# Kernel optimization log

Hardware: AMD Instinct MI355X
Metric: run time of the kernel (lower is better)

## Reference

```python
import jax, jax.numpy as jnp
import numpy as np
import math

NEG = -1000000.0


def setup_inputs() -> dict:
    key = jax.random.key(0)
    ks = jax.random.split(key, 8)
    B, S, D = 4, 2048, 1024
    std = 1.0 / math.sqrt(D)
    return {
        "queries": jax.random.normal(ks[0], (B, S, D), jnp.float32),
        "keys": jax.random.normal(ks[1], (B, S, D), jnp.float32),
        "values": jax.random.normal(ks[2], (B, S, D), jnp.float32),
        "valid_len": jax.random.randint(ks[3], (B,), 1, S, dtype=jnp.int64 if jax.config.jax_enable_x64 else jnp.int32),
        "W_q": jax.random.normal(ks[4], (D, D), jnp.float32) * std,
        "W_k": jax.random.normal(ks[5], (D, D), jnp.float32) * std,
        "W_v": jax.random.normal(ks[6], (D, D), jnp.float32) * std,
        "W_o": jax.random.normal(ks[7], (D, D), jnp.float32) * std,
    }


def reference(queries, keys, values, valid_len, W_q, W_k, W_v, W_o):
    NUM_HEADS = 16
    B, S, D = queries.shape
    hd = D // NUM_HEADS

    def split_heads(x):
        # (B, S, D) -> (B, H, S, hd)
        return x.reshape(B, -1, NUM_HEADS, hd).transpose(0, 2, 1, 3)

    # nn.Linear with weight W applies x @ W.T
    q = split_heads(queries @ W_q.T)
    k = split_heads(keys @ W_k.T)
    v = split_heads(values @ W_v.T)

    scale = 1.0 / math.sqrt(hd)
    scores = jnp.einsum('bhqd,bhkd->bhqk', q, k) * scale  # (B, H, Sq, Sk)

    # key-padding mask from valid_len: positions >= valid_len are masked
    kpos = jnp.arange(scores.shape[-1])
    pad_mask = kpos[None, None, None, :] >= valid_len[:, None, None, None]
    scores = jnp.where(pad_mask, NEG, scores)
    attn = jax.nn.softmax(scores, axis=-1)

    out = jnp.einsum('bhqk,bhkd->bhqd', attn, v)  # (B, H, Sq, hd)
    out = out.transpose(0, 2, 1, 3).reshape(B, -1, D)
    return out @ W_o.T
```

## Files before the change

kernel.cpp:

```cpp
#include <hip/hip_runtime.h>
#include <hip/hip_bf16.h>

using bf16_t = __bf16;
using bf16x8 = __attribute__((ext_vector_type(8))) __bf16;
using bf16x4 = __attribute__((ext_vector_type(4))) __bf16;
using f32x4  = __attribute__((ext_vector_type(4))) float;

#define S_  2048
#define D_  1024

typedef __attribute__((address_space(1))) unsigned int glb_u32;
typedef __attribute__((address_space(3))) unsigned int lds_u32;

__device__ __forceinline__ void async_cp16(const void* g, void* lds) {
    __builtin_amdgcn_global_load_lds(
        (glb_u32*)(unsigned long long)g,
        (lds_u32*)(unsigned int)(unsigned long long)lds,
        16, 0, 0);
}

__global__ __launch_bounds__(256) void cast4_f32_bf16(const float* __restrict__ a, const float* __restrict__ b,
                                                      const float* __restrict__ c, const float* __restrict__ dd,
                                                      bf16_t* __restrict__ oa, bf16_t* __restrict__ ob,
                                                      bf16_t* __restrict__ oc, bf16_t* __restrict__ od, int n4) {
    int i = blockIdx.x * 256 + threadIdx.x;
    if (i >= n4) return;
    const float* s; bf16_t* d;
    int w = blockIdx.y;
    if      (w == 0) { s = a;  d = oa; }
    else if (w == 1) { s = b;  d = ob; }
    else if (w == 2) { s = c;  d = oc; }
    else             { s = dd; d = od; }
    float4 f = reinterpret_cast<const float4*>(s)[i];
    bf16x4 o;
    o[0] = (bf16_t)f.x; o[1] = (bf16_t)f.y; o[2] = (bf16_t)f.z; o[3] = (bf16_t)f.w;
    reinterpret_cast<bf16x4*>(d)[i] = o;
}

__global__ __launch_bounds__(256, 4) void qkv_gemm(const float* __restrict__ qf,
                                                   const float* __restrict__ kf,
                                                   const float* __restrict__ vf,
                                                   const bf16_t* __restrict__ Wqb,
                                                   const bf16_t* __restrict__ Wkb,
                                                   const bf16_t* __restrict__ Wvb,
                                                   bf16_t* __restrict__ Qp,
                                                   bf16_t* __restrict__ Kp,
                                                   bf16_t* __restrict__ Vt,
                                                   float cs) {
    __shared__ bf16_t As[2][128 * 32];
    __shared__ bf16_t Bs[3][128 * 32];
    const int K = 1024;
    int tid  = threadIdx.x;
    int lane = tid & 63;
    int w    = tid >> 6;
    int l15  = lane & 15, quad = lane >> 4;

    int bid = blockIdx.x;
    int xcd = bid & 7, idx = bid >> 3;
    int z   = idx >> 6;
    int rem = idx & 63;
    int m0 = (xcd * 8 + (rem & 7)) * 128;
    int n0 = (rem >> 3) * 128;
    int wm = (w >> 1) * 64, wn = (w & 1) * 64;

    const float*  Af; const bf16_t* Bt;
    if      (z == 0) { Af = qf; Bt = Wqb; }
    else if (z == 1) { Af = kf; Bt = Wkb; }
    else             { Af = vf; Bt = Wvb; }
    float scale = (z == 0) ? cs : 1.0f;

    const float* Ag = Af + (size_t)(m0 + (tid >> 2)) * K + (tid & 3) * 8;

    int arow = tid >> 2, aslot = tid & 3;
    int aoff = arow * 32 + ((aslot ^ ((arow >> 1) & 3)) * 8);

    const bf16_t* bSrc[2]; int bOff[2];
#pragma unroll
    for (int j = 0; j < 2; j++) {
        int linear = j * 256 + tid;
        int row = linear >> 2, s = linear & 3;
        bSrc[j] = Bt + (size_t)(n0 + row) * K + ((s ^ ((row >> 1) & 3)) * 8);
        bOff[j] = linear * 8;
    }

    float4 aE[4], aO[4];
    auto loadA = [&](float4* a, int k0) {
        const float* p = Ag + k0;
        a[0] = *reinterpret_cast<const float4*>(p);
        a[1] = *reinterpret_cast<const float4*>(p + 4);
        a[2] = *reinterpret_cast<const float4*>(p + (size_t)64 * K);
        a[3] = *reinterpret_cast<const float4*>(p + (size_t)64 * K + 4);
    };
    auto storeA = [&](bf16_t* dst, const float4* a) {
        bf16x8 o0, o1;
        o0[0] = (bf16_t)a[0].x; o0[1] = (bf16_t)a[0].y; o0[2] = (bf16_t)a[0].z; o0[3] = (bf16_t)a[0].w;
        o0[4] = (bf16_t)a[1].x; o0[5] = (bf16_t)a[1].y; o0[6] = (bf16_t)a[1].z; o0[7] = (bf16_t)a[1].w;
        o1[0] = (bf16_t)a[2].x; o1[1] = (bf16_t)a[2].y; o1[2] = (bf16_t)a[2].z; o1[3] = (bf16_t)a[2].w;
        o1[4] = (bf16_t)a[3].x; o1[5] = (bf16_t)a[3].y; o1[6] = (bf16_t)a[3].z; o1[7] = (bf16_t)a[3].w;
        *reinterpret_cast<bf16x8*>(dst + aoff)        = o0;
        *reinterpret_cast<bf16x8*>(dst + aoff + 2048) = o1;
    };
    auto stageB = [&](bf16_t* dst, int k0) {
        async_cp16(bSrc[0] + k0, dst + bOff[0]);
        async_cp16(bSrc[1] + k0, dst + bOff[1]);
    };

    f32x4 acc[4][4] = {};
    bf16_t *bRead = Bs[0], *bMid = Bs[1], *bStage = Bs[2];

    loadA(aE, 0);
    stageB(Bs[0], 0);
    loadA(aO, 32);
    stageB(Bs[1], 32);
    storeA(As[0], aE);
    asm volatile("s_waitcnt vmcnt(6) lgkmcnt(0)" ::: "memory");
    __builtin_amdgcn_s_barrier();

#pragma unroll 2
    for (int i = 0; i < 32; ++i) {
        int k2 = (i + 2 < 32) ? (i + 2) * 32 : 992;
        float4* aNew = (i & 1) ? aO : aE;
        loadA(aNew, k2);
        stageB(bStage, k2);

        const bf16_t* Ac = As[i & 1];
        bf16x8 af[4], bfr[4];
#pragma unroll
        for (int t = 0; t < 4; t++) {
            int ra = wm + t * 16 + l15;
            int rb = wn + t * 16 + l15;
            af[t]  = *reinterpret_cast<const bf16x8*>(&Ac[ra * 32 + ((quad ^ ((ra >> 1) & 3)) * 8)]);
            bfr[t] = *reinterpret_cast<const bf16x8*>(&bRead[rb * 32 + ((quad ^ ((rb >> 1) & 3)) * 8)]);
        }
#pragma unroll
        for (int mt = 0; mt < 4; mt++)
#pragma unroll
            for (int nt = 0; nt < 4; nt++)
                acc[mt][nt] = __builtin_amdgcn_mfma_f32_16x16x32_bf16(af[mt], bfr[nt], acc[mt][nt], 0, 0, 0);

        if (i + 1 < 32) storeA(As[(i + 1) & 1], (i & 1) ? aE : aO);

        bf16_t* t0 = bRead; bRead = bMid; bMid = bStage; bStage = t0;
        asm volatile("s_waitcnt vmcnt(6) lgkmcnt(0)" ::: "memory");
        __builtin_amdgcn_s_barrier();
    }

    if (z == 2) {
#pragma unroll
        for (int mt = 0; mt < 4; mt++)
#pragma unroll
            for (int nt = 0; nt < 4; nt++) {
                int m = m0 + wm + mt * 16 + quad * 4;
                int n = n0 + wn + nt * 16 + l15;
                bf16x4 o4;
#pragma unroll
                for (int r = 0; r < 4; r++) o4[r] = (bf16_t)acc[mt][nt][r];
                size_t vrow = (size_t)((m >> 11) * 16 + (n >> 6)) * 64 + (n & 63);
                int ml = m & 2047;
                int mp = (ml & ~31) | (((ml >> 2) & 3) << 3) | (((ml >> 4) & 1) << 2);
                *reinterpret_cast<bf16x4*>(&Vt[vrow * S_ + mp]) = o4;
            }
    } else {
        bf16_t* Co = (z == 0) ? Qp : Kp;
#pragma unroll
        for (int mt = 0; mt < 4; mt++)
#pragma unroll
            for (int nt = 0; nt < 4; nt++)
#pragma unroll
                for (int r = 0; r < 4; r++) {
                    int m = m0 + wm + mt * 16 + quad * 4 + r;
                    int n = n0 + wn + nt * 16 + l15;
                    Co[(size_t)m * 1024 + n] = (bf16_t)(acc[mt][nt][r] * scale);
                }
    }
}

__global__ __launch_bounds__(256) void gemm_out(const bf16_t* __restrict__ A,
                                                const bf16_t* __restrict__ Bt,
                                                float* __restrict__ C) {
    __shared__ bf16_t As[3][128 * 32];
    __shared__ bf16_t Bs[3][128 * 32];
    const int K = 1024;
    int tid  = threadIdx.x;
    int lane = tid & 63;
    int w    = tid >> 6;
    int l15  = lane & 15, quad = lane >> 4;

    int bid = blockIdx.x;
    int xcd = bid & 7, idx = bid >> 3;
    int m0 = (xcd * 8 + (idx & 7)) * 128;
    int n0 = (idx >> 3) * 128;
    int wm = (w >> 1) * 64, wn = (w & 1) * 64;

    const bf16_t* aSrc[2]; const bf16_t* bSrc[2];
    int dOff[2];
#pragma unroll
    for (int j = 0; j < 2; j++) {
        int linear = j * 256 + tid;
        int row = linear >> 2, s = linear & 3;
        int sw = (s ^ ((row >> 1) & 3)) * 8;
        aSrc[j] = A  + (size_t)(m0 + row) * K + sw;
        bSrc[j] = Bt + (size_t)(n0 + row) * K + sw;
        dOff[j] = linear * 8;
    }

    auto stage = [&](int buf, int koff) {
#pragma unroll
        for (int j = 0; j < 2; j++) async_cp16(aSrc[j] + koff, &As[buf][dOff[j]]);
#pragma unroll
        for (int j = 0; j < 2; j++) async_cp16(bSrc[j] + koff, &Bs[buf][dOff[j]]);
    };

    f32x4 acc[4][4] = {};

    stage(0, 0);
    stage(1, 32);

    int cur = 0, nx2 = 2;
    for (int i = 0; i < 32; ++i) {
        if (i == 31) asm volatile("s_waitcnt vmcnt(0)" ::: "memory");
        else         asm volatile("s_waitcnt vmcnt(4)" ::: "memory");
        __builtin_amdgcn_s_barrier();
        if (i + 2 < 32) stage(nx2, (i + 2) * 32);

        bf16x8 af[4], bfr[4];
#pragma unroll
        for (int t = 0; t < 4; t++) {
            int ra = wm + t * 16 + l15;
            int rb = wn + t * 16 + l15;
            af[t]  = *reinterpret_cast<const bf16x8*>(&As[cur][ra * 32 + ((quad ^ ((ra >> 1) & 3)) * 8)]);
            bfr[t] = *reinterpret_cast<const bf16x8*>(&Bs[cur][rb * 32 + ((quad ^ ((rb >> 1) & 3)) * 8)]);
        }
#pragma unroll
        for (int mt = 0; mt < 4; mt++)
#pragma unroll
            for (int nt = 0; nt < 4; nt++)
                acc[mt][nt] = __builtin_amdgcn_mfma_f32_16x16x32_bf16(af[mt], bfr[nt], acc[mt][nt], 0, 0, 0);

        cur = (cur == 2) ? 0 : cur + 1;
        nx2 = (nx2 == 2) ? 0 : nx2 + 1;
    }

#pragma unroll
    for (int mt = 0; mt < 4; mt++)
#pragma unroll
        for (int nt = 0; nt < 4; nt++)
#pragma unroll
            for (int r = 0; r < 4; r++) {
                int m = m0 + wm + mt * 16 + quad * 4 + r;
                int n = n0 + wn + nt * 16 + l15;
                C[(size_t)m * 1024 + n] = acc[mt][nt][r];
            }
}

__global__ __launch_bounds__(256) void attn_fused(const bf16_t* __restrict__ Qp,
                                                  const bf16_t* __restrict__ Kp,
                                                  const bf16_t* __restrict__ Vt,
                                                  const int* __restrict__ vlen_p,
                                                  bf16_t* __restrict__ Out) {
    __shared__ bf16_t smem[4][64 * 64];

    int tid  = threadIdx.x;
    int lane = tid & 63, w = tid >> 6;
    int l15  = lane & 15, quad = lane >> 4;

    int nk[4], ord[4] = {0, 1, 2, 3};
#pragma unroll
    for (int i = 0; i < 4; i++) nk[i] = (vlen_p[i] + 63) >> 6;
#pragma unroll
    for (int i = 0; i < 3; i++)
#pragma unroll
        for (int j = 0; j < 3 - i; j++)
            if (nk[ord[j + 1]] > nk[ord[j]]) { int t = ord[j]; ord[j] = ord[j + 1]; ord[j + 1] = t; }

    int bid  = blockIdx.x;
    int b    = ord[bid >> 9];
    int t    = bid & 511;
    int h    = (t & 7) * 2 + ((t >> 3) & 1);
    int qblk = t >> 4;
    int vlen = vlen_p[b];
    int nkb  = (vlen + 63) >> 6;

    const bf16_t* Qg = Qp + (size_t)(b * S_ + qblk * 64) * D_ + h * 64;
    const bf16_t* Kg = Kp + (size_t)b * S_ * D_ + h * 64;
    const bf16_t* Vg = Vt + (size_t)(b * 16 + h) * 64 * S_;

    int r0 = tid >> 3, s0 = tid & 7;
    int sx = (s0 ^ (r0 & 7)) * 8;
    const bf16_t* kS0 = Kg + (size_t)r0 * D_ + sx;
    const bf16_t* kS1 = kS0 + (size_t)32 * D_;
    const bf16_t* vS0 = Vg + (size_t)r0 * S_ + sx;
    const bf16_t* vS1 = vS0 + (size_t)32 * S_;

    {
        const bf16_t* qS0 = Qg + (size_t)r0 * D_ + sx;
        async_cp16(qS0,                   smem[2] + tid * 8);
        async_cp16(qS0 + (size_t)32 * D_, smem[2] + tid * 8 + 2048);
        async_cp16(kS0, smem[0] + tid * 8);
        async_cp16(kS1, smem[0] + tid * 8 + 2048);
        async_cp16(vS0, smem[1] + tid * 8);
        async_cp16(vS1, smem[1] + tid * 8 + 2048);
    }
    __syncthreads();

    bf16x8 qf[2];
    {
        int row = w * 16 + l15, x = row & 7;
#pragma unroll
        for (int kk = 0; kk < 2; kk++)
            qf[kk] = *reinterpret_cast<const bf16x8*>(&smem[2][row * 64 + ((kk * 4 + quad) ^ x) * 8]);
    }
    __syncthreads();

    f32x4 o[4] = {};
    float l_st = 0.f;

    for (int kb = 0; kb < nkb; kb++) {
        int cur = kb & 1;
        if (kb + 1 < nkb) {
            int nxt = cur ^ 1;
            kS0 += (size_t)64 * D_; kS1 += (size_t)64 * D_;
            vS0 += 64;              vS1 += 64;
            async_cp16(kS0, smem[nxt * 2]     + tid * 8);
            async_cp16(kS1, smem[nxt * 2]     + tid * 8 + 2048);
            async_cp16(vS0, smem[nxt * 2 + 1] + tid * 8);
            async_cp16(vS1, smem[nxt * 2 + 1] + tid * 8 + 2048);
        }
        const bf16_t* Kc = smem[cur * 2];
        const bf16_t* Vc = smem[cur * 2 + 1];

        f32x4 sc[4] = {};
#pragma unroll
        for (int nt = 0; nt < 4; nt++) {
            int row = nt * 16 + l15, x = row & 7;
#pragma unroll
            for (int kk = 0; kk < 2; kk++) {
                bf16x8 kf = *reinterpret_cast<const bf16x8*>(&Kc[row * 64 + ((kk * 4 + quad) ^ x) * 8]);
                sc[nt] = __builtin_amdgcn_mfma_f32_16x16x32_bf16(kf, qf[kk], sc[nt], 0, 0, 0);
            }
        }

        bool partial = (vlen & 63) && (kb == nkb - 1);
        bf16x8 pf[2];
        float lacc = 0.f;
        if (!partial) {
#pragma unroll
            for (int nt = 0; nt < 4; nt++)
#pragma unroll
                for (int r = 0; r < 4; r++) {
                    float p = __builtin_exp2f(sc[nt][r]);
                    lacc += p;
                    pf[nt >> 1][(nt & 1) * 4 + r] = (bf16_t)p;
                }
        } else {
#pragma unroll
            for (int nt = 0; nt < 4; nt++)
#pragma unroll
                for (int r = 0; r < 4; r++) {
                    float p = __builtin_exp2f(sc[nt][r]);
                    if (kb * 64 + nt * 16 + quad * 4 + r >= vlen) p = 0.f;
                    lacc += p;
                    pf[nt >> 1][(nt & 1) * 4 + r] = (bf16_t)p;
                }
        }
        l_st += lacc;

#pragma unroll
        for (int np = 0; np < 2; np++)
#pragma unroll
            for (int dt = 0; dt < 4; dt++) {
                int row = dt * 16 + l15, x = row & 7;
                bf16x8 vfr = *reinterpret_cast<const bf16x8*>(&Vc[row * 64 + ((np * 4 + quad) ^ x) * 8]);
                o[dt] = __builtin_amdgcn_mfma_f32_16x16x32_bf16(vfr, pf[np], o[dt], 0, 0, 0);
            }

        __syncthreads();
    }

    float l = l_st;
    l += __shfl_xor(l, 16);
    l += __shfl_xor(l, 32);
    float inv = 1.0f / l;

    bf16_t* T = smem[0];
    {
        int row = w * 16 + l15, x = row & 7;
#pragma unroll
        for (int dt = 0; dt < 4; dt++) {
            bf16x4 o4;
#pragma unroll
            for (int r = 0; r < 4; r++) o4[r] = (bf16_t)(o[dt][r] * inv);
            int slot = dt * 2 + (quad >> 1);
            *reinterpret_cast<bf16x4*>(&T[row * 64 + (slot ^ x) * 8 + (quad & 1) * 4]) = o4;
        }
    }
    __syncthreads();
    {
        int row = tid >> 2, ch = tid & 3, x = row & 7;
        size_t obase = (size_t)(b * S_ + qblk * 64 + row) * D_ + h * 64 + ch * 16;
        bf16x8 f0 = *reinterpret_cast<const bf16x8*>(&T[row * 64 + ((ch * 2)     ^ x) * 8]);
        bf16x8 f1 = *reinterpret_cast<const bf16x8*>(&T[row * 64 + ((ch * 2 + 1) ^ x) * 8]);
        *reinterpret_cast<bf16x8*>(&Out[obase])     = f0;
        *reinterpret_cast<bf16x8*>(&Out[obase + 8]) = f1;
    }
}

extern "C" void kernel_launch(void* const* d_in, const int* in_sizes, int n_in,
                              void* d_out, int out_size, void* d_ws, size_t ws_size,
                              hipStream_t stream) {
    const float* q  = (const float*)d_in[0];
    const float* k  = (const float*)d_in[1];
    const float* v  = (const float*)d_in[2];
    const int*   vl = (const int*)d_in[3];
    const float* Wq = (const float*)d_in[4];
    const float* Wk = (const float*)d_in[5];
    const float* Wv = (const float*)d_in[6];
    const float* Wo = (const float*)d_in[7];
    float* out = (float*)d_out;

    bf16_t* ws = (bf16_t*)d_ws;
    const size_t SD = (size_t)8192 * 1024;
    const size_t WW = (size_t)1024 * 1024;
    bf16_t* tmpB = ws + SD;
    bf16_t* Qp   = ws + 2 * SD;
    bf16_t* Kp   = ws + 3 * SD;
    bf16_t* Vt   = ws + 4 * SD;
    bf16_t* Wqb  = ws + 5 * SD;
    bf16_t* Wkb  = Wqb + WW;
    bf16_t* Wvb  = Wqb + 2 * WW;
    bf16_t* Wob  = Wqb + 3 * WW;

    const float cs = 0.18033688f;
    dim3 blk(256);

    cast4_f32_bf16<<<dim3(1024, 4), blk, 0, stream>>>(Wq, Wk, Wv, Wo, Wqb, Wkb, Wvb, Wob, 262144);
    qkv_gemm<<<dim3(1536), blk, 0, stream>>>(q, k, v, Wqb, Wkb, Wvb, Qp, Kp, Vt, cs);
    attn_fused<<<dim3(2048), blk, 0, stream>>>(Qp, Kp, Vt, vl, tmpB);
    gemm_out<<<dim3(512), blk, 0, stream>>>(tmpB, Wob, out);
}
```

Before: 311.9 us.

## Pre-cast activations to bf16 and use 256x256-tile 8-wave GEMMs for projections

Adds a separate kernel that casts the q/k/v activations to bf16 up front. The QKV and output projections then run through a new 256x256-tile, 512-thread GEMM with async global-to-LDS double buffering, split K halves, barriers interleaved with MFMA phases, and raised wave priority during MFMA. The goal is more data reuse per tile and better overlap of loads with MFMA than the old fp32-loading 128x128 QKV GEMM. The cost is an extra activation cast pass with its own memory traffic, a larger workspace requirement, and far fewer blocks (384 and 128), which may leave some compute units idle. The old path is kept as a fallback when the workspace is too small.

Measured after the change: 319.9 us. 2.5% more time.

```diff
diff --git a/kernel.cpp b/kernel.cpp
--- a/kernel.cpp
+++ b/kernel.cpp
@@ -35,6 +35,214 @@
     bf16x4 o;
     o[0] = (bf16_t)f.x; o[1] = (bf16_t)f.y; o[2] = (bf16_t)f.z; o[3] = (bf16_t)f.w;
     reinterpret_cast<bf16x4*>(d)[i] = o;
+}
+
+__global__ __launch_bounds__(256) void cast3_f32_bf16(const float* __restrict__ q, const float* __restrict__ k,
+                                                      const float* __restrict__ v,
+                                                      bf16_t* __restrict__ oq, bf16_t* __restrict__ ok,
+                                                      bf16_t* __restrict__ ov, int n4) {
+    int i = blockIdx.x * 256 + threadIdx.x;
+    if (i >= n4) return;
+    const float* s; bf16_t* d;
+    int w = blockIdx.y;
+    if      (w == 0) { s = q; d = oq; }
+    else if (w == 1) { s = k; d = ok; }
+    else             { s = v; d = ov; }
+    float4 f = reinterpret_cast<const float4*>(s)[i];
+    bf16x4 o;
+    o[0] = (bf16_t)f.x; o[1] = (bf16_t)f.y; o[2] = (bf16_t)f.z; o[3] = (bf16_t)f.w;
+    reinterpret_cast<bf16x4*>(d)[i] = o;
+}
+
+template <int MODE>
+__global__ __launch_bounds__(512, 2) void gemm8(const bf16_t* __restrict__ Aq,
+                                                const bf16_t* __restrict__ Ak,
+                                                const bf16_t* __restrict__ Av,
+                                                const bf16_t* __restrict__ Wq,
+                                                const bf16_t* __restrict__ Wk,
+                                                const bf16_t* __restrict__ Wv,
+                                                bf16_t* __restrict__ Qp,
+                                                bf16_t* __restrict__ Kp,
+                                                bf16_t* __restrict__ Vt,
+                                                float cs,
+                                                float* __restrict__ Co) {
+    __shared__ bf16_t As[2][2][256 * 32];
+    __shared__ bf16_t Bs[2][2][256 * 32];
+    const int K = 1024;
+    constexpr int NKT = 16;
+    int tid  = threadIdx.x;
+    int lane = tid & 63, w = tid >> 6;
+    int l15  = lane & 15, quad = lane >> 4;
+    int wr = w >> 2, wc = w & 3;
+
+    int bid = blockIdx.x;
+    int xcd = bid & 7, r = bid >> 3;
+    int z = 0, r2 = r;
+    if (MODE == 0) { z = r >> 4; r2 = r & 15; }
+    int m0 = (xcd * 4 + (r2 & 3)) * 256;
+    int n0 = (r2 >> 2) * 256;
+
+    const bf16_t *Ag, *Bg;
+    if (MODE == 0) {
+        Ag = (z == 0) ? Aq : (z == 1) ? Ak : Av;
+        Bg = (z == 0) ? Wq : (z == 1) ? Wk : Wv;
+    } else { Ag = Aq; Bg = Wq; }
+
+    const bf16_t* aS[2]; const bf16_t* bS[2]; int ldOff[2];
+#pragma unroll
+    for (int j = 0; j < 2; j++) {
+        int c = j * 512 + tid;
+        int row = c >> 2, s = c & 3;
+        int ks = (s ^ ((row >> 1) & 3)) * 8;
+        aS[j] = Ag + (size_t)(m0 + row) * K + ks;
+        bS[j] = Bg + (size_t)(n0 + row) * K + ks;
+        ldOff[j] = c * 8;
+    }
+    auto stage = [&](int buf, int t, int half) {
+        int kh = half >> 1;
+        int koff = t * 64 + kh * 32;
+        if ((half & 1) == 0) {
+            async_cp16(aS[0] + koff, &As[buf][kh][ldOff[0]]);
+            async_cp16(aS[1] + koff, &As[buf][kh][ldOff[1]]);
+        } else {
+            async_cp16(bS[0] + koff, &Bs[buf][kh][ldOff[0]]);
+            async_cp16(bS[1] + koff, &Bs[buf][kh][ldOff[1]]);
+        }
+    };
+
+    int aoff[8], boff[4];
+#pragma unroll
+    for (int i = 0; i < 8; i++) {
+        int row = wr * 128 + i * 16 + l15;
+        aoff[i] = row * 32 + ((quad ^ ((row >> 1) & 3)) * 8);
+    }
+#pragma unroll
+    for (int jn = 0; jn < 4; jn++) {
+        int row = wc * 64 + jn * 16 + l15;
+        boff[jn] = row * 32 + ((quad ^ ((row >> 1) & 3)) * 8);
+    }
+
+    f32x4 acc[8][4] = {};
+
+    stage(0, 0, 0); stage(0, 0, 1); stage(0, 0, 2); stage(0, 0, 3);
+    asm volatile("s_waitcnt vmcnt(4)" ::: "memory");
+    __builtin_amdgcn_s_barrier();
+
+    for (int t = 0; t < NKT; ++t) {
+        int buf = t & 1, nbuf = buf ^ 1;
+        bool st = (t + 1 < NKT);
+        const bf16_t* A0 = As[buf][0]; const bf16_t* A1 = As[buf][1];
+        const bf16_t* B0 = Bs[buf][0]; const bf16_t* B1 = Bs[buf][1];
+        bf16x8 af[4], bfr[4];
+
+#pragma unroll
+        for (int i = 0; i < 4; i++) af[i] = *reinterpret_cast<const bf16x8*>(&A0[aoff[i]]);
+#pragma unroll
+        for (int jn = 0; jn < 4; jn++) bfr[jn] = *reinterpret_cast<const bf16x8*>(&B0[boff[jn]]);
+        if (st) stage(nbuf, t + 1, 0);
+        __builtin_amdgcn_s_barrier();
+        asm volatile("s_waitcnt lgkmcnt(0)" ::: "memory");
+        __builtin_amdgcn_sched_barrier(0);
+        __builtin_amdgcn_s_setprio(1);
+#pragma unroll
+        for (int i = 0; i < 4; i++)
+#pragma unroll
+            for (int jn = 0; jn < 4; jn++)
+                acc[i][jn] = __builtin_amdgcn_mfma_f32_16x16x32_bf16(af[i], bfr[jn], acc[i][jn], 0, 0, 0);
+        __builtin_amdgcn_s_setprio(0);
+        __builtin_amdgcn_s_barrier();
+
+#pragma unroll
+        for (int i = 0; i < 4; i++) af[i] = *reinterpret_cast<const bf16x8*>(&A0[aoff[4 + i]]);
+        if (st) stage(nbuf, t + 1, 1);
+        __builtin_amdgcn_s_barrier();
+        asm volatile("s_waitcnt lgkmcnt(0)" ::: "memory");
+        __builtin_amdgcn_sched_barrier(0);
+        __builtin_amdgcn_s_setprio(1);
+#pragma unroll
+        for (int i = 0; i < 4; i++)
+#pragma unroll
+            for (int jn = 0; jn < 4; jn++)
+                acc[4 + i][jn] = __builtin_amdgcn_mfma_f32_16x16x32_bf16(af[i], bfr[jn], acc[4 + i][jn], 0, 0, 0);
+        __builtin_amdgcn_s_setprio(0);
+        if (t == NKT - 1) asm volatile("s_waitcnt vmcnt(0)" ::: "memory");
+        else              asm volatile("s_waitcnt vmcnt(4)" ::: "memory");
+        __builtin_amdgcn_s_barrier();
+
+#pragma unroll
+        for (int i = 0; i < 4; i++) af[i] = *reinterpret_cast<const bf16x8*>(&A1[aoff[i]]);
+#pragma unroll
+        for (int jn = 0; jn < 4; jn++) bfr[jn] = *reinterpret_cast<const bf16x8*>(&B1[boff[jn]]);
+        if (st) stage(nbuf, t + 1, 2);
+        __builtin_amdgcn_s_barrier();
+        asm volatile("s_waitcnt lgkmcnt(0)" ::: "memory");
+        __builtin_amdgcn_sched_barrier(0);
+        __builtin_amdgcn_s_setprio(1);
+#pragma unroll
+        for (int i = 0; i < 4; i++)
+#pragma unroll
+            for (int jn = 0; jn < 4; jn++)
+                acc[i][jn] = __builtin_amdgcn_mfma_f32_16x16x32_bf16(af[i], bfr[jn], acc[i][jn], 0, 0, 0);
+        __builtin_amdgcn_s_setprio(0);
+        __builtin_amdgcn_s_barrier();
+
+#pragma unroll
+        for (int i = 0; i < 4; i++) af[i] = *reinterpret_cast<const bf16x8*>(&A1[aoff[4 + i]]);
+        if (st) stage(nbuf, t + 1, 3);
+        __builtin_amdgcn_s_barrier();
+        asm volatile("s_waitcnt lgkmcnt(0)" ::: "memory");
+        __builtin_amdgcn_sched_barrier(0);
+        __builtin_amdgcn_s_setprio(1);
+#pragma unroll
+        for (int i = 0; i < 4; i++)
+#pragma unroll
+            for (int jn = 0; jn < 4; jn++)
+                acc[4 + i][jn] = __builtin_amdgcn_mfma_f32_16x16x32_bf16(af[i], bfr[jn], acc[4 + i][jn], 0, 0, 0);
+        __builtin_amdgcn_s_setprio(0);
+        asm volatile("s_waitcnt vmcnt(4)" ::: "memory");
+        __builtin_amdgcn_s_barrier();
+    }
+
+    if (MODE == 0 && z == 2) {
+#pragma unroll
+        for (int i = 0; i < 8; i++)
+#pragma unroll
+            for (int jn = 0; jn < 4; jn++) {
+                int m = m0 + wr * 128 + i * 16 + quad * 4;
+                int n = n0 + wc * 64 + jn * 16 + l15;
+                bf16x4 o4;
+#pragma unroll
+                for (int rr = 0; rr < 4; rr++) o4[rr] = (bf16_t)acc[i][jn][rr];
+                size_t vrow = (size_t)((m >> 11) * 16 + (n >> 6)) * 64 + (n & 63);
+                int ml = m & 2047;
+                int mp = (ml & ~31) | (((ml >> 2) & 3) << 3) | (((ml >> 4) & 1) << 2);
+                *reinterpret_cast<bf16x4*>(&Vt[vrow * S_ + mp]) = o4;
+            }
+    } else if (MODE == 0) {
+        bf16_t* CoH = (z == 0) ? Qp : Kp;
+        float scale = (z == 0) ? cs : 1.0f;
+#pragma unroll
+        for (int i = 0; i < 8; i++)
+#pragma unroll
+            for (int jn = 0; jn < 4; jn++)
+#pragma unroll
+                for (int rr = 0; rr < 4; rr++) {
+                    int m = m0 + wr * 128 + i * 16 + quad * 4 + rr;
+                    int n = n0 + wc * 64 + jn * 16 + l15;
+                    CoH[(size_t)m * 1024 + n] = (bf16_t)(acc[i][jn][rr] * scale);
+                }
+    } else {
+#pragma unroll
+        for (int i = 0; i < 8; i++)
+#pragma unroll
+            for (int jn = 0; jn < 4; jn++)
+#pragma unroll
+                for (int rr = 0; rr < 4; rr++) {
+                    int m = m0 + wr * 128 + i * 16 + quad * 4 + rr;
+                    int n = n0 + wc * 64 + jn * 16 + l15;
+                    Co[(size_t)m * 1024 + n] = acc[i][jn][rr];
+                }
+    }
 }
 
 __global__ __launch_bounds__(256, 4) void qkv_gemm(const float* __restrict__ qf,
@@ -70,7 +278,6 @@
     float scale = (z == 0) ? cs : 1.0f;
 
     const float* Ag = Af + (size_t)(m0 + (tid >> 2)) * K + (tid & 3) * 8;
-
     int arow = tid >> 2, aslot = tid & 3;
     int aoff = arow * 32 + ((aslot ^ ((arow >> 1) & 3)) * 8);
 
@@ -175,84 +382,6 @@
     }
 }
 
-__global__ __launch_bounds__(256) void gemm_out(const bf16_t* __restrict__ A,
-                                                const bf16_t* __restrict__ Bt,
-                                                float* __restrict__ C) {
-    __shared__ bf16_t As[3][128 * 32];
-    __shared__ bf16_t Bs[3][128 * 32];
-    const int K = 1024;
-    int tid  = threadIdx.x;
-    int lane = tid & 63;
-    int w    = tid >> 6;
-    int l15  = lane & 15, quad = lane >> 4;
-
-    int bid = blockIdx.x;
-    int xcd = bid & 7, idx = bid >> 3;
-    int m0 = (xcd * 8 + (idx & 7)) * 128;
-    int n0 = (idx >> 3) * 128;
-    int wm = (w >> 1) * 64, wn = (w & 1) * 64;
-
-    const bf16_t* aSrc[2]; const bf16_t* bSrc[2];
-    int dOff[2];
-#pragma unroll
-    for (int j = 0; j < 2; j++) {
-        int linear = j * 256 + tid;
-        int row = linear >> 2, s = linear & 3;
-        int sw = (s ^ ((row >> 1) & 3)) * 8;
-        aSrc[j] = A  + (size_t)(m0 + row) * K + sw;
-        bSrc[j] = Bt + (size_t)(n0 + row) * K + sw;
-        dOff[j] = linear * 8;
-    }
-
-    auto stage = [&](int buf, int koff) {
-#pragma unroll
-        for (int j = 0; j < 2; j++) async_cp16(aSrc[j] + koff, &As[buf][dOff[j]]);
-#pragma unroll
-        for (int j = 0; j < 2; j++) async_cp16(bSrc[j] + koff, &Bs[buf][dOff[j]]);
-    };
-
-    f32x4 acc[4][4] = {};
-
-    stage(0, 0);
-    stage(1, 32);
-
-    int cur = 0, nx2 = 2;
-    for (int i = 0; i < 32; ++i) {
-        if (i == 31) asm volatile("s_waitcnt vmcnt(0)" ::: "memory");
-        else         asm volatile("s_waitcnt vmcnt(4)" ::: "memory");
-        __builtin_amdgcn_s_barrier();
-        if (i + 2 < 32) stage(nx2, (i + 2) * 32);
-
-        bf16x8 af[4], bfr[4];
-#pragma unroll
-        for (int t = 0; t < 4; t++) {
-            int ra = wm + t * 16 + l15;
-            int rb = wn + t * 16 + l15;
-            af[t]  = *reinterpret_cast<const bf16x8*>(&As[cur][ra * 32 + ((quad ^ ((ra >> 1) & 3)) * 8)]);
-            bfr[t] = *reinterpret_cast<const bf16x8*>(&Bs[cur][rb * 32 + ((quad ^ ((rb >> 1) & 3)) * 8)]);
-        }
-#pragma unroll
-        for (int mt = 0; mt < 4; mt++)
-#pragma unroll
-            for (int nt = 0; nt < 4; nt++)
-                acc[mt][nt] = __builtin_amdgcn_mfma_f32_16x16x32_bf16(af[mt], bfr[nt], acc[mt][nt], 0, 0, 0);
-
-        cur = (cur == 2) ? 0 : cur + 1;
-        nx2 = (nx2 == 2) ? 0 : nx2 + 1;
-    }
-
-#pragma unroll
-    for (int mt = 0; mt < 4; mt++)
-#pragma unroll
-        for (int nt = 0; nt < 4; nt++)
-#pragma unroll
-            for (int r = 0; r < 4; r++) {
-                int m = m0 + wm + mt * 16 + quad * 4 + r;
-                int n = n0 + wn + nt * 16 + l15;
-                C[(size_t)m * 1024 + n] = acc[mt][nt][r];
-            }
-}
-
 __global__ __launch_bounds__(256) void attn_fused(const bf16_t* __restrict__ Qp,
                                                   const bf16_t* __restrict__ Kp,
                                                   const bf16_t* __restrict__ Vt,
@@ -405,6 +534,84 @@
     }
 }
 
+__global__ __launch_bounds__(256) void gemm_out(const bf16_t* __restrict__ A,
+                                                const bf16_t* __restrict__ Bt,
+                                                float* __restrict__ C) {
+    __shared__ bf16_t As[3][128 * 32];
+    __shared__ bf16_t Bs[3][128 * 32];
+    const int K = 1024;
+    int tid  = threadIdx.x;
+    int lane = tid & 63;
+    int w    = tid >> 6;
+    int l15  = lane & 15, quad = lane >> 4;
+
+    int bid = blockIdx.x;
+    int xcd = bid & 7, idx = bid >> 3;
+    int m0 = (xcd * 8 + (idx & 7)) * 128;
+    int n0 = (idx >> 3) * 128;
+    int wm = (w >> 1) * 64, wn = (w & 1) * 64;
+
+    const bf16_t* aSrc[2]; const bf16_t* bSrc[2];
+    int dOff[2];
+#pragma unroll
+    for (int j = 0; j < 2; j++) {
+        int linear = j * 256 + tid;
+        int row = linear >> 2, s = linear & 3;
+        int sw = (s ^ ((row >> 1) & 3)) * 8;
+        aSrc[j] = A  + (size_t)(m0 + row) * K + sw;
+        bSrc[j] = Bt + (size_t)(n0 + row) * K + sw;
+        dOff[j] = linear * 8;
+    }
+
+    auto stage = [&](int buf, int koff) {
+#pragma unroll
+        for (int j = 0; j < 2; j++) async_cp16(aSrc[j] + koff, &As[buf][dOff[j]]);
+#pragma unroll
+        for (int j = 0; j < 2; j++) async_cp16(bSrc[j] + koff, &Bs[buf][dOff[j]]);
+    };
+
+    f32x4 acc[4][4] = {};
+
+    stage(0, 0);
+    stage(1, 32);
+
+    int cur = 0, nx2 = 2;
+    for (int i = 0; i < 32; ++i) {
+        if (i == 31) asm volatile("s_waitcnt vmcnt(0)" ::: "memory");
+        else         asm volatile("s_waitcnt vmcnt(4)" ::: "memory");
+        __builtin_amdgcn_s_barrier();
+        if (i + 2 < 32) stage(nx2, (i + 2) * 32);
+
+        bf16x8 af[4], bfr[4];
+#pragma unroll
+        for (int t = 0; t < 4; t++) {
+            int ra = wm + t * 16 + l15;
+            int rb = wn + t * 16 + l15;
+            af[t]  = *reinterpret_cast<const bf16x8*>(&As[cur][ra * 32 + ((quad ^ ((ra >> 1) & 3)) * 8)]);
+            bfr[t] = *reinterpret_cast<const bf16x8*>(&Bs[cur][rb * 32 + ((quad ^ ((rb >> 1) & 3)) * 8)]);
+        }
+#pragma unroll
+        for (int mt = 0; mt < 4; mt++)
+#pragma unroll
+            for (int nt = 0; nt < 4; nt++)
+                acc[mt][nt] = __builtin_amdgcn_mfma_f32_16x16x32_bf16(af[mt], bfr[nt], acc[mt][nt], 0, 0, 0);
+
+        cur = (cur == 2) ? 0 : cur + 1;
+        nx2 = (nx2 == 2) ? 0 : nx2 + 1;
+    }
+
+#pragma unroll
+    for (int mt = 0; mt < 4; mt++)
+#pragma unroll
+        for (int nt = 0; nt < 4; nt++)
+#pragma unroll
+            for (int r = 0; r < 4; r++) {
+                int m = m0 + wm + mt * 16 + quad * 4 + r;
+                int n = n0 + wn + nt * 16 + l15;
+                C[(size_t)m * 1024 + n] = acc[mt][nt][r];
+            }
+}
+
 extern "C" void kernel_launch(void* const* d_in, const int* in_sizes, int n_in,
                               void* d_out, int out_size, void* d_ws, size_t ws_size,
                               hipStream_t stream) {
@@ -421,20 +628,41 @@
     bf16_t* ws = (bf16_t*)d_ws;
     const size_t SD = (size_t)8192 * 1024;
     const size_t WW = (size_t)1024 * 1024;
-    bf16_t* tmpB = ws + SD;
-    bf16_t* Qp   = ws + 2 * SD;
-    bf16_t* Kp   = ws + 3 * SD;
-    bf16_t* Vt   = ws + 4 * SD;
-    bf16_t* Wqb  = ws + 5 * SD;
-    bf16_t* Wkb  = Wqb + WW;
-    bf16_t* Wvb  = Wqb + 2 * WW;
-    bf16_t* Wob  = Wqb + 3 * WW;
-
     const float cs = 0.18033688f;
     dim3 blk(256);
 
-    cast4_f32_bf16<<<dim3(1024, 4), blk, 0, stream>>>(Wq, Wk, Wv, Wo, Wqb, Wkb, Wvb, Wob, 262144);
-    qkv_gemm<<<dim3(1536), blk, 0, stream>>>(q, k, v, Wqb, Wkb, Wvb, Qp, Kp, Vt, cs);
-    attn_fused<<<dim3(2048), blk, 0, stream>>>(Qp, Kp, Vt, vl, tmpB);
-    gemm_out<<<dim3(512), blk, 0, stream>>>(tmpB, Wob, out);
-}
+    size_t need = (6 * SD + 4 * WW) * sizeof(bf16_t);
+    if (ws_size >= need) {
+        bf16_t* qb  = ws;
+        bf16_t* kb  = ws + SD;
+        bf16_t* vb  = ws + 2 * SD;
+        bf16_t* Qp  = ws + 3 * SD;
+        bf16_t* Kp  = ws + 4 * SD;
+        bf16_t* Vt  = ws + 5 * SD;
+        bf16_t* Wqb = ws + 6 * SD;
+        bf16_t* Wkb = Wqb + WW;
+        bf16_t* Wvb = Wqb + 2 * WW;
+        bf16_t* Wob = Wqb + 3 * WW;
+
+        cast4_f32_bf16<<<dim3(1024, 4), blk, 0, stream>>>(Wq, Wk, Wv, Wo, Wqb, Wkb, Wvb, Wob, 262144);
+        cast3_f32_bf16<<<dim3(8192, 3), blk, 0, stream>>>(q, k, v, qb, kb, vb, 2097152);
+        gemm8<0><<<dim3(384), dim3(512), 0, stream>>>(qb, kb, vb, Wqb, Wkb, Wvb, Qp, Kp, Vt, cs, nullptr);
+        attn_fused<<<dim3(2048), blk, 0, stream>>>(Qp, Kp, Vt, vl, qb);
+        gemm8<1><<<dim3(128), dim3(512), 0, stream>>>(qb, nullptr, nullptr, Wob, nullptr, nullptr,
+                                                      nullptr, nullptr, nullptr, 1.0f, out);
+    } else {
+        bf16_t* tmpB = ws + SD;
+        bf16_t* Qp   = ws + 2 * SD;
+        bf16_t* Kp   = ws + 3 * SD;
+        bf16_t* Vt   = ws + 4 * SD;
+        bf16_t* Wqb  = ws + 5 * SD;
+        bf16_t* Wkb  = Wqb + WW;
+        bf16_t* Wvb  = Wqb + 2 * WW;
+        bf16_t* Wob  = Wqb + 3 * WW;
+
+        cast4_f32_bf16<<<dim3(1024, 4), blk, 0, stream>>>(Wq, Wk, Wv, Wo, Wqb, Wkb, Wvb, Wob, 262144);
+        qkv_gemm<<<dim3(1536), blk, 0, stream>>>(q, k, v, Wqb, Wkb, Wvb, Qp, Kp, Vt, cs);
+        attn_fused<<<dim3(2048), blk, 0, stream>>>(Qp, Kp, Vt, vl, tmpB);
+        gemm_out<<<dim3(512), blk, 0, stream>>>(tmpB, Wob, out);
+    }
+}
```
